# Kernel tuning notes

Measured on AMD Instinct MI355X. Metric: run time of the kernel, lower is better.

The kernel has to match this reference:

```python
import jax, jax.numpy as jnp
import numpy as np

IMG_H = 800
IMG_W = 800
LEVEL_HW = [(200, 200), (100, 100), (50, 50), (25, 25), (13, 13)]
SIZES = [32.0, 64.0, 128.0, 256.0, 512.0]
RATIOS = np.array([0.5, 1.0, 2.0])
PRE_NMS = 1000     # rpn_pre_nms_top_n_test
POST_NMS = 1000    # rpn_post_nms_top_n_test
NMS_THRESH = 0.7
MIN_SIZE = 1e-3
BBOX_CLAMP = float(np.log(1000.0 / 16.0))  # torchvision BoxCoder clamp


def _make_anchors():
    """torchvision AnchorGenerator: 3 anchors/location, (h,w,a)-major order."""
    per_level = []
    for (H, W), size in zip(LEVEL_HW, SIZES):
        h_r = np.sqrt(RATIOS)
        w_r = 1.0 / h_r
        ws = w_r * size
        hs = h_r * size
        base = np.round(np.stack([-ws, -hs, ws, hs], axis=1) / 2.0)  # [3,4]
        stride_y = IMG_H // H
        stride_x = IMG_W // W
        shift_x = np.arange(W) * stride_x
        shift_y = np.arange(H) * stride_y
        yy, xx = np.meshgrid(shift_y, shift_x, indexing='ij')
        shifts = np.stack([xx.ravel(), yy.ravel(), xx.ravel(), yy.ravel()], axis=1)
        a = (shifts[:, None, :] + base[None, :, :]).reshape(-1, 4)  # [H*W*3,4]
        per_level.append(jnp.asarray(a, jnp.float32))
    return per_level


def _conv(x, w, b, pad):
    y = jax.lax.conv_general_dilated(
        x, w, window_strides=(1, 1), padding=[(pad, pad), (pad, pad)],
        dimension_numbers=('NCHW', 'OIHW', 'NCHW'))
    return y + b[None, :, None, None]


def _rpn_forward(feats, conv_w, conv_b, cls_w, cls_b, bbox_w, bbox_b):
    anchors_l = _make_anchors()
    boxes_list, scores_list, lvls_list = [], [], []
    for lvl, f in enumerate(feats):
        t = jax.nn.relu(_conv(f, conv_w, conv_b, 1))
        logits = _conv(t, cls_w, cls_b, 0)     # [1,3,H,W]
        deltas = _conv(t, bbox_w, bbox_b, 0)   # [1,12,H,W]
        H, W = f.shape[2], f.shape[3]
        s = logits[0].transpose(1, 2, 0).reshape(-1)                       # (h,w,a)
        d = deltas[0].reshape(3, 4, H, W).transpose(2, 3, 0, 1).reshape(-1, 4)
        k = min(PRE_NMS, s.shape[0])
        topv, topi = jax.lax.top_k(s, k)
        a = anchors_l[lvl][topi]
        dd = d[topi]
        # BoxCoder.decode, weights=(1,1,1,1)
        w_ = a[:, 2] - a[:, 0]
        h_ = a[:, 3] - a[:, 1]
        cx = a[:, 0] + 0.5 * w_
        cy = a[:, 1] + 0.5 * h_
        dx, dy = dd[:, 0], dd[:, 1]
        dw = jnp.minimum(dd[:, 2], BBOX_CLAMP)
        dh = jnp.minimum(dd[:, 3], BBOX_CLAMP)
        pcx = dx * w_ + cx
        pcy = dy * h_ + cy
        pw = jnp.exp(dw) * w_
        ph = jnp.exp(dh) * h_
        bx = jnp.stack([pcx - 0.5 * pw, pcy - 0.5 * ph,
                        pcx + 0.5 * pw, pcy + 0.5 * ph], axis=1)
        boxes_list.append(bx)
        scores_list.append(topv)
        lvls_list.append(jnp.full((k,), float(lvl), jnp.float32))
    boxes = jnp.concatenate(boxes_list)    # [N,4], N=4507
    scores = jnp.concatenate(scores_list)
    lvls = jnp.concatenate(lvls_list)
    # clip to image
    boxes = jnp.stack([boxes[:, 0].clip(0.0, IMG_W), boxes[:, 1].clip(0.0, IMG_H),
                       boxes[:, 2].clip(0.0, IMG_W), boxes[:, 3].clip(0.0, IMG_H)], axis=1)
    valid = ((boxes[:, 2] - boxes[:, 0]) >= MIN_SIZE) & ((boxes[:, 3] - boxes[:, 1]) >= MIN_SIZE)
    # batched NMS: offset boxes per level so cross-level IoU is zero
    off = lvls * (IMG_W + 1.0)
    ob = boxes + off[:, None]
    N = boxes.shape[0]
    order = jnp.argsort(-scores)
    b = ob[order]
    rb = boxes[order]
    s = scores[order]
    v = valid[order]
    area = (b[:, 2] - b[:, 0]) * (b[:, 3] - b[:, 1])
    lt = jnp.maximum(b[:, None, :2], b[None, :, :2])
    rbr = jnp.minimum(b[:, None, 2:], b[None, :, 2:])
    wh = jnp.clip(rbr - lt, 0.0)
    inter = wh[..., 0] * wh[..., 1]
    iou = inter / (area[:, None] + area[None, :] - inter)  # [N,N]
    idxs = jnp.arange(N)
    def body(i, keep):
        sup = keep[i] & (iou[i] > NMS_THRESH) & (idxs > i)
        return keep & ~sup
    keep = jax.lax.fori_loop(0, N, body, v)
    final_scores = jnp.where(keep, s, -jnp.inf)
    _, ki = jax.lax.top_k(final_scores, POST_NMS)
    return rb[ki]  # [POST_NMS, 4] proposals (padded to fixed size)


def setup_inputs() -> dict:
    key = jax.random.key(0)
    ks = jax.random.split(key, 12)
    inp = {}
    for i, (name, (H, W)) in enumerate(zip(['feat0', 'feat1', 'feat2', 'feat3', 'feat4'], LEVEL_HW)):
        inp[name] = jax.random.normal(ks[i], (1, 256, H, W), jnp.float32)
    inp['conv_w'] = jax.random.normal(ks[5], (256, 256, 3, 3), jnp.float32) * 0.02
    inp['conv_b'] = jnp.zeros((256,), jnp.float32)
    inp['cls_w'] = jax.random.normal(ks[6], (3, 256, 1, 1), jnp.float32) * 0.02
    inp['cls_b'] = jnp.zeros((3,), jnp.float32)
    inp['bbox_w'] = jax.random.normal(ks[7], (12, 256, 1, 1), jnp.float32) * 0.02
    inp['bbox_b'] = jnp.zeros((12,), jnp.float32)
    return inp


def reference(feat0, feat1, feat2, feat3, feat4, conv_w, conv_b, cls_w, cls_b, bbox_w, bbox_b):
    feats = [feat0, feat1, feat2, feat3, feat4]
    return _rpn_forward(feats, conv_w, conv_b, cls_w, cls_b, bbox_w, bbox_b)
```

## Files before the change

kernel.cpp:

```cpp
#include <hip/hip_runtime.h>
#include <cmath>

typedef unsigned int u32;
typedef unsigned long long u64;
typedef _Float16 f16;
typedef _Float16 f16x8 __attribute__((ext_vector_type(8)));
typedef float f32x4 __attribute__((ext_vector_type(4)));

typedef __attribute__((address_space(1))) const unsigned int gu32;
typedef __attribute__((address_space(3))) unsigned int lu32;

#define NCAND 4507
#define WORDS 71
#define ROWS_AL (WORDS * 64)
#define TOTS 159882
#define NTILES 863
#define CONVGRID 512

__constant__ int c_W[5]      = {200, 100, 50, 25, 13};
__constant__ int c_stride[5] = {4, 8, 16, 32, 61};
__constant__ int c_Nl[5]     = {120000, 30000, 7500, 1875, 507};
__constant__ int c_soff[5]   = {0, 120000, 150000, 157500, 159375};
__constant__ int c_k[5]      = {1000, 1000, 1000, 1000, 507};

__constant__ int cv_boff[6]  = {0, 625, 794, 843, 859, 863};

struct DecParams { float b[5][3][4]; };
struct FeatPtrs { const float* p[5]; };

__device__ __forceinline__ u32 flipf(float f) {
    u32 u = __float_as_uint(f);
    return (u & 0x80000000u) ? ~u : (u | 0x80000000u);
}

constexpr size_t AL(size_t x) { return (x + 255) & ~(size_t)255; }
constexpr size_t OFF_WHI    = 0;
constexpr size_t OFF_WLO    = AL(OFF_WHI + 1179648);
constexpr size_t OFF_HEADW  = AL(OFF_WLO + 1179648);
constexpr size_t OFF_HEADB  = AL(OFF_HEADW + 3840 * 4);
constexpr size_t OFF_SCORES = AL(OFF_HEADB + 64);
constexpr size_t OFF_DELTAS = AL(OFF_SCORES + (size_t)TOTS * 4);
constexpr size_t OFF_SBOX   = AL(OFF_DELTAS + (size_t)TOTS * 16);
constexpr size_t OFF_SOB    = AL(OFF_SBOX + (size_t)NCAND * 16);
constexpr size_t OFF_SVAL   = AL(OFF_SOB + (size_t)NCAND * 16);
constexpr size_t OFF_MASK   = AL(OFF_SVAL + (size_t)NCAND * 4);
constexpr size_t OFF_KEEP   = AL(OFF_MASK + (size_t)ROWS_AL * WORDS * 8);
constexpr size_t OFF_GHIST  = AL(OFF_KEEP + WORDS * 8);
constexpr size_t OFF_CNT    = AL(OFF_GHIST + 1280 * 4);
constexpr size_t OFF_KEY    = AL(OFF_CNT + 64);

__global__ __launch_bounds__(256) void k_prep(
    const float* __restrict__ cw, const float* __restrict__ clsw,
    const float* __restrict__ clsb, const float* __restrict__ bw,
    const float* __restrict__ bb, f16* __restrict__ whi, f16* __restrict__ wlo,
    float* __restrict__ headw, float* __restrict__ headb,
    u32* __restrict__ ghist, u32* __restrict__ cnts) {
    int i = blockIdx.x * 256 + threadIdx.x;
    if (i < 589824) {
        int blk = i >> 13;
        int within = i & 8191;
        int co = within >> 5;
        int rem = within & 31;
        int slot = rem >> 3, j = rem & 7;
        int chunk = blk / 9, kk = blk - chunk * 9;
        int ky = kk / 3, kx = kk - ky * 3;
        int g = slot ^ ((co >> 1) & 3);
        int ci = (chunk << 5) | (g << 3) | j;
        float w = cw[(((co << 8) + ci) * 3 + ky) * 3 + kx];
        f16 hi = (f16)w;
        whi[i] = hi;
        wlo[i] = (f16)((w - (float)hi) * 2048.0f);
    }
    if (i < 3840) {
        int h = i >> 8, ci = i & 255;
        headw[i] = (h < 3) ? clsw[h * 256 + ci] : bw[(h - 3) * 256 + ci];
    }
    if (i < 15) headb[i] = (i < 3) ? clsb[i] : bb[i - 3];
    if (i < 1280) ghist[i] = 0;
    if (i < 16) cnts[i] = 0;
}

__global__ __launch_bounds__(512) void k_conv(
    FeatPtrs fp, const f16* __restrict__ whi, const f16* __restrict__ wlo,
    const float* __restrict__ convb, const float* __restrict__ headw,
    const float* __restrict__ headb, float* __restrict__ scores,
    float* __restrict__ deltas, u32* __restrict__ ghist) {
    __shared__ float4 smq[4896];
    char* smb = (char*)smq;
    const int tid = threadIdx.x;
    const int lane = tid & 63, wv = tid >> 6;
    const int l15 = lane & 15, l4 = lane >> 4;

    int rbase0, rbase1, rbase2, rbase3;
    {
        int rr = l15 >> 3;
        rbase0 = (0 + rr) * 640; rbase1 = (2 + rr) * 640;
        rbase2 = (4 + rr) * 640; rbase3 = (6 + rr) * 640;
    }
    int colx0, colx1, colx2;
    {
        int c = lane & 7;
        int p0 = c, p1 = c + 1, p2 = c + 2;
        colx0 = p0 * 64 + ((l4 ^ ((p0 >> 1) & 3)) << 4);
        colx1 = p1 * 64 + ((l4 ^ ((p1 >> 1) & 3)) << 4);
        colx2 = p2 * 64 + ((l4 ^ ((p2 >> 1) & 3)) << 4);
    }
    const int bco0 = wv * 32 + l15, bco1 = wv * 32 + 16 + l15;
    const int boff0 = bco0 * 64 + ((l4 ^ ((bco0 >> 1) & 3)) << 4);
    const int boff1 = bco1 * 64 + ((l4 ^ ((bco1 >> 1) & 3)) << 4);

    for (int bt = blockIdx.x; bt < NTILES; bt += gridDim.x) {
        int l = 0;
#pragma unroll
        for (int q = 1; q < 5; q++) if (bt >= cv_boff[q]) l = q;
        const int H = c_W[l], W = H;
        const int soff = c_soff[l];
        const float* __restrict__ in = fp.p[l];
        const int t = bt - cv_boff[l];
        const int tilesx = (W + 7) >> 3;
        const int tx = t % tilesx, ty = t / tilesx;
        const int x0 = tx * 8, y0 = ty * 8;
        const int HW = H * W;

        f32x4 acc1[4][2], acc2[4][2];
#pragma unroll
        for (int mt = 0; mt < 4; mt++)
#pragma unroll
            for (int nt = 0; nt < 2; nt++) {
                acc1[mt][nt] = (f32x4)0.0f;
                acc2[mt][nt] = (f32x4)0.0f;
            }

        auto stagePatch = [&](int chunk) {
            const int c0 = chunk << 5;
            f16* ph = (f16*)smb;
            f16* pl = (f16*)(smb + 6400);
            for (int e = tid; e < 3200; e += 512) {
                int py = e / 320, rem = e - py * 320;
                int px = rem >> 5, ci = rem & 31;
                int gy = y0 - 1 + py, gx = x0 - 1 + px;
                float v = 0.f;
                if (gy >= 0 && gy < H && gx >= 0 && gx < W)
                    v = in[(c0 + ci) * HW + gy * W + gx];
                f16 hi = (f16)v;
                int widx = py * 320 + px * 32 + (((ci >> 3) ^ ((px >> 1) & 3)) << 3) + (ci & 7);
                ph[widx] = hi;
                pl[widx] = (f16)((v - (float)hi) * 2048.0f);
            }
        };
        auto issueB = [&](int sidx, int buf) {
            const char* gh = (const char*)whi + (size_t)sidx * 16384;
            const char* gl = (const char*)wlo + (size_t)sidx * 16384;
            char* dh = smb + 12800 + buf * 32768;
            char* dl = dh + 16384;
#pragma unroll
            for (int q = 0; q < 2; q++) {
                int i1 = (wv * 2 + q) * 1024;
                __builtin_amdgcn_global_load_lds((gu32*)(gh + i1 + lane * 16), (lu32*)(dh + i1), 16, 0, 0);
                __builtin_amdgcn_global_load_lds((gu32*)(gl + i1 + lane * 16), (lu32*)(dl + i1), 16, 0, 0);
            }
        };

        stagePatch(0);
        issueB(0, 0);
        __syncthreads();

        for (int chunk = 0; chunk < 8; ++chunk) {
            if (chunk) { stagePatch(chunk); __syncthreads(); }
#pragma unroll
            for (int kk = 0; kk < 9; ++kk) {
                const int s = chunk * 9 + kk;
                const int buf = s & 1;
                if (s < 71) issueB(s + 1, buf ^ 1);
                {
                    const int ky = kk / 3, kx = kk - ky * 3;
                    const int kyb = ky * 640;
                    const int cx = (kx == 0) ? colx0 : (kx == 1) ? colx1 : colx2;
                    const char* bh = smb + 12800 + buf * 32768;
                    const char* bl = bh + 16384;
                    f16x8 ah0 = *(const f16x8*)(smb + rbase0 + kyb + cx);
                    f16x8 ah1 = *(const f16x8*)(smb + rbase1 + kyb + cx);
                    f16x8 ah2 = *(const f16x8*)(smb + rbase2 + kyb + cx);
                    f16x8 ah3 = *(const f16x8*)(smb + rbase3 + kyb + cx);
                    f16x8 al0 = *(const f16x8*)(smb + 6400 + rbase0 + kyb + cx);
                    f16x8 al1 = *(const f16x8*)(smb + 6400 + rbase1 + kyb + cx);
                    f16x8 al2 = *(const f16x8*)(smb + 6400 + rbase2 + kyb + cx);
                    f16x8 al3 = *(const f16x8*)(smb + 6400 + rbase3 + kyb + cx);
#pragma unroll
                    for (int nt = 0; nt < 2; nt++) {
                        const int bo = nt ? boff1 : boff0;
                        f16x8 vbh = *(const f16x8*)(bh + bo);
                        f16x8 vbl = *(const f16x8*)(bl + bo);
                        acc1[0][nt] = __builtin_amdgcn_mfma_f32_16x16x32_f16(ah0, vbh, acc1[0][nt], 0, 0, 0);
                        acc2[0][nt] = __builtin_amdgcn_mfma_f32_16x16x32_f16(ah0, vbl, acc2[0][nt], 0, 0, 0);
                        acc2[0][nt] = __builtin_amdgcn_mfma_f32_16x16x32_f16(al0, vbh, acc2[0][nt], 0, 0, 0);
                        acc1[1][nt] = __builtin_amdgcn_mfma_f32_16x16x32_f16(ah1, vbh, acc1[1][nt], 0, 0, 0);
                        acc2[1][nt] = __builtin_amdgcn_mfma_f32_16x16x32_f16(ah1, vbl, acc2[1][nt], 0, 0, 0);
                        acc2[1][nt] = __builtin_amdgcn_mfma_f32_16x16x32_f16(al1, vbh, acc2[1][nt], 0, 0, 0);
                        acc1[2][nt] = __builtin_amdgcn_mfma_f32_16x16x32_f16(ah2, vbh, acc1[2][nt], 0, 0, 0);
                        acc2[2][nt] = __builtin_amdgcn_mfma_f32_16x16x32_f16(ah2, vbl, acc2[2][nt], 0, 0, 0);
                        acc2[2][nt] = __builtin_amdgcn_mfma_f32_16x16x32_f16(al2, vbh, acc2[2][nt], 0, 0, 0);
                        acc1[3][nt] = __builtin_amdgcn_mfma_f32_16x16x32_f16(ah3, vbh, acc1[3][nt], 0, 0, 0);
                        acc2[3][nt] = __builtin_amdgcn_mfma_f32_16x16x32_f16(ah3, vbl, acc2[3][nt], 0, 0, 0);
                        acc2[3][nt] = __builtin_amdgcn_mfma_f32_16x16x32_f16(al3, vbh, acc2[3][nt], 0, 0, 0);
                    }
                }
                __syncthreads();
            }
        }

        const float INV2048 = 4.8828125e-4f;
        {
            float cb0 = convb[bco0], cb1 = convb[bco1];
#pragma unroll
            for (int mt = 0; mt < 4; mt++)
#pragma unroll
                for (int nt = 0; nt < 2; nt++) {
                    float cb = nt ? cb1 : cb0;
#pragma unroll
                    for (int r = 0; r < 4; r++) {
                        float tv = acc1[mt][nt][r] + acc2[mt][nt][r] * INV2048 + cb;
                        acc1[mt][nt][r] = tv > 0.f ? tv : 0.f;
                    }
                }
        }

        u32* lhist = (u32*)(smb + 12800);
        for (int i = tid; i < 1280; i += 512) lhist[i] = 0;

        float* part = (float*)smb;
        for (int hc = 0; hc < 15; hc += 3) {
            float hw3[3][2];
#pragma unroll
            for (int h3 = 0; h3 < 3; h3++) {
                hw3[h3][0] = headw[(hc + h3) * 256 + bco0];
                hw3[h3][1] = headw[(hc + h3) * 256 + bco1];
            }
#pragma unroll
            for (int mt = 0; mt < 4; mt++)
#pragma unroll
                for (int r = 0; r < 4; r++) {
                    float p0 = 0.f, p1 = 0.f, p2 = 0.f;
#pragma unroll
                    for (int nt = 0; nt < 2; nt++) {
                        float tv = acc1[mt][nt][r];
                        p0 = fmaf(hw3[0][nt], tv, p0);
                        p1 = fmaf(hw3[1][nt], tv, p1);
                        p2 = fmaf(hw3[2][nt], tv, p2);
                    }
                    p0 += __shfl_xor(p0, 1); p0 += __shfl_xor(p0, 2); p0 += __shfl_xor(p0, 4); p0 += __shfl_xor(p0, 8);
                    p1 += __shfl_xor(p1, 1); p1 += __shfl_xor(p1, 2); p1 += __shfl_xor(p1, 4); p1 += __shfl_xor(p1, 8);
                    p2 += __shfl_xor(p2, 1); p2 += __shfl_xor(p2, 2); p2 += __shfl_xor(p2, 4); p2 += __shfl_xor(p2, 8);
                    if (l15 == 0) {
                        int px = mt * 16 + l4 * 4 + r;
                        part[(wv * 64 + px) * 3 + 0] = p0;
                        part[(wv * 64 + px) * 3 + 1] = p1;
                        part[(wv * 64 + px) * 3 + 2] = p2;
                    }
                }
            __syncthreads();
            if (tid < 192) {
                int px = tid / 3, h3 = tid % 3;
                int h = hc + h3;
                float sum = 0.f;
#pragma unroll
                for (int g = 0; g < 8; g++) sum += part[(g * 64 + px) * 3 + h3];
                sum += headb[h];
                int gy = y0 + (px >> 3), gx = x0 + (px & 7);
                if (gy < H && gx < W) {
                    int pix = gy * W + gx;
                    if (h < 3) {
                        scores[soff + pix * 3 + h] = sum;
                        atomicAdd(&lhist[l * 256 + (flipf(sum) >> 24)], 1u);
                    } else {
                        int ch2 = h - 3;
                        deltas[((size_t)(soff + pix * 3 + (ch2 >> 2))) * 4 + (ch2 & 3)] = sum;
                    }
                }
            }
            __syncthreads();
        }
        for (int i = tid; i < 1280; i += 512) {
            u32 v = lhist[i];
            if (v) atomicAdd(&ghist[i], v);
        }
        __syncthreads();
    }
}

__global__ __launch_bounds__(1024) void k_clsfin(
    const float* __restrict__ scores, const u32* __restrict__ ghist,
    u64* __restrict__ key, u64* __restrict__ scr1, u64* __restrict__ scr2,
    u32* __restrict__ cnts, const float* __restrict__ deltas, DecParams P,
    float* __restrict__ sboxes, float* __restrict__ sob, u32* __restrict__ svalid) {
    __shared__ u64 sk[8192];
    __shared__ u32 lh[1280];
    __shared__ u32 tiebuf[2048];
    __shared__ u32 sb0[5];
    __shared__ u32 sh_sel, sh_t1, sh_t2, sh_m, sh_last;
    const int tid = threadIdx.x;
    const int lane = tid & 63;

    for (int i = tid; i < 1280; i += 1024) lh[i] = ghist[i];
    __syncthreads();
    if (tid < 4) {
        int l = tid;
        u32 m0 = (u32)c_k[l];
        u32 cum = 0;
        for (int b = 255; b >= 0; --b) {
            u32 c = lh[l * 256 + b];
            if (cum + c >= m0) { sb0[l] = (u32)b; break; }
            cum += c;
        }
    }
    __syncthreads();
    const int gsz = gridDim.x * 1024;
    for (int i = blockIdx.x * 1024 + tid; i < TOTS; i += gsz) {
        int l = (i >= 120000) + (i >= 150000) + (i >= 157500) + (i >= 159375);
        u32 il = (u32)(i - c_soff[l]);
        u32 k32 = flipf(scores[i]);
        u32 b = k32 >> 24;
        bool sel = (l == 4) || (b > sb0[l]);
        bool tie = (l < 4) && (b == sb0[l]);
        u64 m1 = __ballot(sel);
        while (m1) {
            int ldr = __builtin_ctzll(m1);
            int lv = __shfl(l, ldr);
            u64 grp = __ballot(sel && (l == lv));
            u32 bs = 0;
            if (lane == ldr) bs = atomicAdd(&cnts[lv], (u32)__popcll(grp));
            bs = __shfl(bs, ldr);
            if (sel && l == lv) {
                u32 slot = bs + (u32)__popcll(grp & ((1ull << lane) - 1ull));
                key[lv * 1000 + slot] = ((u64)(~k32) << 32) | (u64)(((u32)lv << 24) | il);
            }
            m1 &= ~grp;
        }
        u64 m2 = __ballot(tie);
        while (m2) {
            int ldr = __builtin_ctzll(m2);
            int lv = __shfl(l, ldr);
            u64 grp = __ballot(tie && (l == lv));
            u32 bs = 0;
            if (lane == ldr) bs = atomicAdd(&cnts[8 + lv], (u32)__popcll(grp));
            bs = __shfl(bs, ldr);
            if (tie && l == lv) {
                u32 slot = bs + (u32)__popcll(grp & ((1ull << lane) - 1ull));
                scr1[c_soff[lv] + slot] = ((u64)k32 << 32) | (u64)il;
            }
            m2 &= ~grp;
        }
    }
    __threadfence();
    if (tid == 0) sh_last = (atomicAdd(&cnts[12], 1u) == gridDim.x - 1) ? 1u : 0u;
    __syncthreads();
    if (!sh_last) return;
    __threadfence();

    u32* hist = lh;
    for (int l = 0; l < 5; ++l) {
        u32 n = cnts[l];
        int base = l * 1000;
        for (u32 j = tid; j < n; j += 1024) sk[base + j] = key[base + j];
    }
    __syncthreads();
    for (int l = 0; l < 4; ++l) {
        const int off = c_soff[l], base = l * 1000;
        const u32 lshift = (u32)l << 24;
        u32 nsel = cnts[l];
        u32 m = (u32)c_k[l] - nsel;
        u32 n = cnts[8 + l];
        u64* curb = scr1 + off;
        u64* nxtb = scr2 + off;
        if (tid == 0) sh_sel = nsel;
        __syncthreads();
        for (int p = 1; p <= 3; ++p) {
            if (n == m) break;
            const int shift = 56 - 8 * p;
            for (int b = tid; b < 256; b += 1024) hist[b] = 0;
            if (tid == 0) sh_t1 = 0;
            __syncthreads();
            for (u32 j = tid; j < n; j += 1024)
                atomicAdd(&hist[(u32)(curb[j] >> shift) & 255u], 1u);
            __syncthreads();
            if (tid == 0) {
                u32 cum = 0;
                for (int b = 255; b >= 0; --b) {
                    u32 c = hist[b];
                    if (cum + c >= m) { sh_t2 = (u32)b; sh_m = m - cum; break; }
                    cum += c;
                }
            }
            __syncthreads();
            u32 bp = sh_t2; m = sh_m;
            for (u32 j = tid; j < n; j += 1024) {
                u64 e = curb[j];
                u32 b = (u32)(e >> shift) & 255u;
                bool sel = b > bp, tie = (b == bp);
                u64 msk = __ballot(sel);
                if (msk) {
                    int ldr = __builtin_ctzll(msk);
                    u32 bs = 0;
                    if (lane == ldr) bs = atomicAdd(&sh_sel, (u32)__popcll(msk));
                    bs = __shfl(bs, ldr);
                    if (sel) {
                        u32 slot = bs + (u32)__popcll(msk & ((1ull << lane) - 1ull));
                        u32 k32 = (u32)(e >> 32);
                        sk[base + slot] = ((u64)(~k32) << 32) | (u64)(lshift | (u32)(e & 0xFFFFFFu));
                    }
                }
                msk = __ballot(tie);
                if (msk) {
                    int ldr = __builtin_ctzll(msk);
                    u32 bs = 0;
                    if (lane == ldr) bs = atomicAdd(&sh_t1, (u32)__popcll(msk));
                    bs = __shfl(bs, ldr);
                    if (tie) {
                        u32 slot = bs + (u32)__popcll(msk & ((1ull << lane) - 1ull));
                        nxtb[slot] = e;
                    }
                }
            }
            __syncthreads();
            n = sh_t1;
            __syncthreads();
            u64* tmp = curb; curb = nxtb; nxtb = tmp;
        }
        u32 cs = sh_sel;
        if (n == m) {
            for (u32 j = tid; j < n; j += 1024) {
                u64 e = curb[j];
                u32 k32 = (u32)(e >> 32);
                sk[base + cs + j] = ((u64)(~k32) << 32) | (u64)(lshift | (u32)(e & 0xFFFFFFu));
            }
        } else {
            u32 kt = (u32)(curb[0] >> 32);
            u32 nc = n > 2048u ? 2048u : n;
            u32 S = 64; while (S < nc) S <<= 1;
            for (u32 j = tid; j < S; j += 1024) tiebuf[j] = 0xFFFFFFFFu;
            __syncthreads();
            for (u32 j = tid; j < nc; j += 1024) tiebuf[j] = (u32)(curb[j] & 0xFFFFFFu);
            __syncthreads();
            for (u32 ksz = 2; ksz <= S; ksz <<= 1) {
                for (u32 jj = ksz >> 1; jj > 0; jj >>= 1) {
                    for (u32 i2 = tid; i2 < S; i2 += 1024) {
                        u32 ixj = i2 ^ jj;
                        if (ixj > i2) {
                            u32 a = tiebuf[i2], b2 = tiebuf[ixj];
                            bool up = ((i2 & ksz) == 0);
                            if ((a > b2) == up) { tiebuf[i2] = b2; tiebuf[ixj] = a; }
                        }
                    }
                    __syncthreads();
                }
            }
            for (u32 j = tid; j < m; j += 1024)
                sk[base + cs + j] = ((u64)(~kt) << 32) | (u64)(lshift | tiebuf[j]);
        }
        __syncthreads();
    }
    for (int i = tid; i < 8192; i += 1024) if (i >= NCAND) sk[i] = ~0ull;
    __syncthreads();
    for (u32 ksz = 2; ksz <= 8192; ksz <<= 1) {
        for (u32 j = ksz >> 1; j > 0; j >>= 1) {
            for (u32 i = tid; i < 8192; i += 1024) {
                u32 ixj = i ^ j;
                if (ixj > i) {
                    u64 a = sk[i], b = sk[ixj];
                    bool up = ((i & ksz) == 0);
                    if ((a > b) == up) { sk[i] = b; sk[ixj] = a; }
                }
            }
            __syncthreads();
        }
    }
    const float CLAMP = 4.135166556742356f;
    for (int s = tid; s < NCAND; s += 1024) {
        u32 info = (u32)sk[s];
        int l = info >> 24, idx = info & 0xFFFFFF;
        int W = c_W[l], st = c_stride[l];
        int a = idx % 3, pix = idx / 3;
        int x = pix % W, y = pix / W;
        float ax1 = x * st + P.b[l][a][0];
        float ay1 = y * st + P.b[l][a][1];
        float ax2 = x * st + P.b[l][a][2];
        float ay2 = y * st + P.b[l][a][3];
        float w_ = ax2 - ax1, h_ = ay2 - ay1;
        float cx = ax1 + 0.5f * w_, cy = ay1 + 0.5f * h_;
        const float* d = deltas + ((size_t)(c_soff[l] + idx)) * 4;
        float dx = d[0], dy = d[1];
        float dw = fminf(d[2], CLAMP), dh = fminf(d[3], CLAMP);
        float pcx = dx * w_ + cx, pcy = dy * h_ + cy;
        float pw = expf(dw) * w_, ph = expf(dh) * h_;
        float x1 = pcx - 0.5f * pw, y1 = pcy - 0.5f * ph;
        float x2 = pcx + 0.5f * pw, y2 = pcy + 0.5f * ph;
        x1 = fminf(fmaxf(x1, 0.f), 800.f); y1 = fminf(fmaxf(y1, 0.f), 800.f);
        x2 = fminf(fmaxf(x2, 0.f), 800.f); y2 = fminf(fmaxf(y2, 0.f), 800.f);
        u32 vv = (x2 - x1 >= 0.001f && y2 - y1 >= 0.001f) ? 1u : 0u;
        float offv = (float)l * 801.0f;
        sboxes[s * 4 + 0] = x1; sboxes[s * 4 + 1] = y1;
        sboxes[s * 4 + 2] = x2; sboxes[s * 4 + 3] = y2;
        sob[s * 4 + 0] = x1 + offv; sob[s * 4 + 1] = y1 + offv;
        sob[s * 4 + 2] = x2 + offv; sob[s * 4 + 3] = y2 + offv;
        svalid[s] = vv;
    }
}

__global__ __launch_bounds__(1024) void k_maskscan(
    const float* __restrict__ sob, u64* __restrict__ mask,
    const u32* __restrict__ svalid, const float* __restrict__ sboxes,
    float* __restrict__ out, u32* __restrict__ cnts) {
    __shared__ u64 stage[2][64][WORDS];
    __shared__ u64 keep[WORDS];
    __shared__ u32 ormL[WORDS], ormH[WORDS];
    __shared__ u32 sc[1024];
    __shared__ u32 sh_last;
    const int tid = threadIdx.x;
    int gid = blockIdx.x * 1024 + tid;
    const int total = NCAND * WORDS;
    if (gid < total) {
        int i = gid / WORDS, w = gid - i * WORDS;
        float bx1 = sob[i * 4], by1 = sob[i * 4 + 1], bx2 = sob[i * 4 + 2], by2 = sob[i * 4 + 3];
        float ai = (bx2 - bx1) * (by2 - by1);
        u64 bits = 0;
        int j0 = w * 64;
        for (int b = 0; b < 64; b++) {
            int j = j0 + b;
            if (j < NCAND && j > i) {
                float cx1 = sob[j * 4], cy1 = sob[j * 4 + 1], cx2 = sob[j * 4 + 2], cy2 = sob[j * 4 + 3];
                float lt0 = fmaxf(bx1, cx1), lt1 = fmaxf(by1, cy1);
                float rb0 = fminf(bx2, cx2), rb1 = fminf(by2, cy2);
                float ww = fmaxf(rb0 - lt0, 0.f), hh = fmaxf(rb1 - lt1, 0.f);
                float inter = ww * hh;
                float aj = (cx2 - cx1) * (cy2 - cy1);
                float u = ai + aj - inter;
                float iou = inter / u;
                if (iou > 0.7f) bits |= (1ull << b);
            }
        }
        mask[(size_t)i * WORDS + w] = bits;
    }
    __threadfence();
    if (tid == 0) sh_last = (atomicAdd(&cnts[13], 1u) == gridDim.x - 1) ? 1u : 0u;
    __syncthreads();
    if (!sh_last) return;
    __threadfence();

    if (tid < WORDS) {
        u64 w0 = 0;
        for (int b = 0; b < 64; b++) {
            int idx = tid * 64 + b;
            if (idx < NCAND && svalid[idx]) w0 |= (1ull << b);
        }
        keep[tid] = w0; ormL[tid] = 0; ormH[tid] = 0;
    }
    {
        u64* s0 = &stage[0][0][0];
        for (int e = tid; e < 64 * WORDS; e += 1024) {
            int r = e / WORDS, w = e - r * WORDS;
            s0[e] = (r < NCAND) ? mask[(size_t)r * WORDS + w] : 0ull;
        }
    }
    __syncthreads();

    for (int t = 0; t < WORDS; t++) {
        const int cur = t & 1;
        u64 pf[5];
        if (t < WORDS - 1) {
            int row0 = (t + 1) * 64;
#pragma unroll
            for (int q = 0; q < 5; q++) {
                int e = tid + q * 1024;
                u64 v = 0;
                if (e < 64 * WORDS) {
                    int r = e / WORDS, w = e - r * WORDS;
                    int row = row0 + r;
                    if (row < NCAND) v = mask[(size_t)row * WORDS + w];
                }
                pf[q] = v;
            }
        }
        if (tid < 64) {
            u64 d = stage[cur][tid][t];
            u64 nz = __ballot(d != 0ull);
            u64 curk = keep[t];
            u64 pending = curk & nz;
            while (pending) {
                int b = __builtin_ctzll(pending);
                pending &= pending - 1;
                u64 mb = stage[cur][b][t];
                curk &= ~mb;
                pending &= ~mb;
            }
            if (tid == 0) keep[t] = curk;
        }
        __syncthreads();
        u64 kw = keep[t];
        int nW = WORDS - 1 - t;
        for (int task = tid; task < 64 * nW; task += 1024) {
            int r = task / nW, w = t + 1 + (task - r * nW);
            if ((kw >> r) & 1ull) {
                u64 mrow = stage[cur][r][w];
                if (mrow) {
                    atomicOr(&ormL[w], (u32)mrow);
                    atomicOr(&ormH[w], (u32)(mrow >> 32));
                }
            }
        }
        __syncthreads();
        if (tid > t && tid < WORDS) {
            keep[tid] &= ~(((u64)ormH[tid] << 32) | (u64)ormL[tid]);
            ormL[tid] = 0; ormH[tid] = 0;
        }
        if (t < WORDS - 1) {
            u64* s1 = &stage[cur ^ 1][0][0];
#pragma unroll
            for (int q = 0; q < 5; q++) {
                int e = tid + q * 1024;
                if (e < 64 * WORDS) s1[e] = pf[q];
            }
        }
        __syncthreads();
    }
    const int i0 = tid * 5;
    u32 cnt = 0;
    for (int e = 0; e < 5; e++) {
        int i = i0 + e;
        if (i < NCAND) cnt += (u32)((keep[i >> 6] >> (i & 63)) & 1ull);
    }
    sc[tid] = cnt;
    __syncthreads();
    for (int off = 1; off < 1024; off <<= 1) {
        u32 v = (tid >= off) ? sc[tid - off] : 0;
        __syncthreads();
        sc[tid] += v;
        __syncthreads();
    }
    u32 incl = sc[tid];
    u32 totalk = sc[1023];
    u32 kr = incl - cnt;
    for (int e = 0; e < 5; e++) {
        int i = i0 + e;
        if (i < NCAND) {
            bool kp = (keep[i >> 6] >> (i & 63)) & 1ull;
            if (kp) {
                if (kr < 1000u) {
                    out[kr * 4 + 0] = sboxes[i * 4 + 0];
                    out[kr * 4 + 1] = sboxes[i * 4 + 1];
                    out[kr * 4 + 2] = sboxes[i * 4 + 2];
                    out[kr * 4 + 3] = sboxes[i * 4 + 3];
                }
                kr++;
            } else {
                u32 slot = totalk + (u32)i - kr;
                if (slot < 1000u) {
                    out[slot * 4 + 0] = sboxes[i * 4 + 0];
                    out[slot * 4 + 1] = sboxes[i * 4 + 1];
                    out[slot * 4 + 2] = sboxes[i * 4 + 2];
                    out[slot * 4 + 3] = sboxes[i * 4 + 3];
                }
            }
        }
    }
}

extern "C" void kernel_launch(void* const* d_in, const int* in_sizes, int n_in,
                              void* d_out, int out_size, void* d_ws, size_t ws_size,
                              hipStream_t stream) {
    (void)in_sizes; (void)n_in; (void)out_size; (void)ws_size;
    FeatPtrs fp;
    for (int i = 0; i < 5; i++) fp.p[i] = (const float*)d_in[i];
    const float* conv_w = (const float*)d_in[5];
    const float* conv_b = (const float*)d_in[6];
    const float* cls_w  = (const float*)d_in[7];
    const float* cls_b  = (const float*)d_in[8];
    const float* bbox_w = (const float*)d_in[9];
    const float* bbox_b = (const float*)d_in[10];

    char* ws = (char*)d_ws;
    f16*   whi    = (f16*)(ws + OFF_WHI);
    f16*   wlo    = (f16*)(ws + OFF_WLO);
    float* headw  = (float*)(ws + OFF_HEADW);
    float* headb  = (float*)(ws + OFF_HEADB);
    float* scores = (float*)(ws + OFF_SCORES);
    float* deltas = (float*)(ws + OFF_DELTAS);
    float* sboxes = (float*)(ws + OFF_SBOX);
    float* sob    = (float*)(ws + OFF_SOB);
    u32*   svalid = (u32*)(ws + OFF_SVAL);
    u64*   maskp  = (u64*)(ws + OFF_MASK);
    u32*   ghist  = (u32*)(ws + OFF_GHIST);
    u32*   cnts   = (u32*)(ws + OFF_CNT);
    u64*   key    = (u64*)(ws + OFF_KEY);
    u64*   scr1   = maskp;
    u64*   scr2   = maskp + TOTS;

    k_prep<<<2304, 256, 0, stream>>>(conv_w, cls_w, cls_b, bbox_w, bbox_b,
                                     whi, wlo, headw, headb, ghist, cnts);

    k_conv<<<CONVGRID, 512, 0, stream>>>(fp, whi, wlo, conv_b, headw, headb,
                                         scores, deltas, ghist);

    DecParams dp;
    {
        const double sz[5] = {32.0, 64.0, 128.0, 256.0, 512.0};
        const double rt[3] = {0.5, 1.0, 2.0};
        for (int l = 0; l < 5; l++)
            for (int a = 0; a < 3; a++) {
                double hr = sqrt(rt[a]);
                double wr = 1.0 / hr;
                double w = wr * sz[l], h = hr * sz[l];
                dp.b[l][a][0] = (float)nearbyint(-w / 2.0);
                dp.b[l][a][1] = (float)nearbyint(-h / 2.0);
                dp.b[l][a][2] = (float)nearbyint(w / 2.0);
                dp.b[l][a][3] = (float)nearbyint(h / 2.0);
            }
    }
    k_clsfin<<<128, 1024, 0, stream>>>(scores, ghist, key, scr1, scr2, cnts,
                                       deltas, dp, sboxes, sob, svalid);
    k_maskscan<<<(NCAND * WORDS + 1023) / 1024, 1024, 0, stream>>>(
        sob, maskp, svalid, sboxes, (float*)d_out, cnts);
}
```

Measured before the change: 820.0 us.

## Read conv weight fragments directly from global memory instead of LDS double buffer

Removes the async global-to-LDS double-buffered weight staging and instead has each lane load its B fragments straight from global memory, likely served by cache. This shrinks LDS from about 78KB to about 12.8KB, which could allow more blocks per CU, and drops the per-tap barrier. In exchange every wave issues redundant global loads for the same weight slices, and load latency is no longer hidden by prefetch. The histogram scratch is moved to fit the smaller LDS allocation.

```diff
diff --git a/kernel.cpp b/kernel.cpp
--- a/kernel.cpp
+++ b/kernel.cpp
@@ -6,9 +6,6 @@
 typedef _Float16 f16;
 typedef _Float16 f16x8 __attribute__((ext_vector_type(8)));
 typedef float f32x4 __attribute__((ext_vector_type(4)));
-
-typedef __attribute__((address_space(1))) const unsigned int gu32;
-typedef __attribute__((address_space(3))) unsigned int lu32;
 
 #define NCAND 4507
 #define WORDS 71
@@ -85,7 +82,7 @@
     const float* __restrict__ convb, const float* __restrict__ headw,
     const float* __restrict__ headb, float* __restrict__ scores,
     float* __restrict__ deltas, u32* __restrict__ ghist) {
-    __shared__ float4 smq[4896];
+    __shared__ float4 smq[804];
     char* smb = (char*)smq;
     const int tid = threadIdx.x;
     const int lane = tid & 63, wv = tid >> 6;
@@ -148,64 +145,45 @@
                 pl[widx] = (f16)((v - (float)hi) * 2048.0f);
             }
         };
-        auto issueB = [&](int sidx, int buf) {
-            const char* gh = (const char*)whi + (size_t)sidx * 16384;
-            const char* gl = (const char*)wlo + (size_t)sidx * 16384;
-            char* dh = smb + 12800 + buf * 32768;
-            char* dl = dh + 16384;
-#pragma unroll
-            for (int q = 0; q < 2; q++) {
-                int i1 = (wv * 2 + q) * 1024;
-                __builtin_amdgcn_global_load_lds((gu32*)(gh + i1 + lane * 16), (lu32*)(dh + i1), 16, 0, 0);
-                __builtin_amdgcn_global_load_lds((gu32*)(gl + i1 + lane * 16), (lu32*)(dl + i1), 16, 0, 0);
-            }
-        };
-
-        stagePatch(0);
-        issueB(0, 0);
-        __syncthreads();
 
         for (int chunk = 0; chunk < 8; ++chunk) {
-            if (chunk) { stagePatch(chunk); __syncthreads(); }
+            __syncthreads();
+            stagePatch(chunk);
+            __syncthreads();
 #pragma unroll
             for (int kk = 0; kk < 9; ++kk) {
                 const int s = chunk * 9 + kk;
-                const int buf = s & 1;
-                if (s < 71) issueB(s + 1, buf ^ 1);
-                {
-                    const int ky = kk / 3, kx = kk - ky * 3;
-                    const int kyb = ky * 640;
-                    const int cx = (kx == 0) ? colx0 : (kx == 1) ? colx1 : colx2;
-                    const char* bh = smb + 12800 + buf * 32768;
-                    const char* bl = bh + 16384;
-                    f16x8 ah0 = *(const f16x8*)(smb + rbase0 + kyb + cx);
-                    f16x8 ah1 = *(const f16x8*)(smb + rbase1 + kyb + cx);
-                    f16x8 ah2 = *(const f16x8*)(smb + rbase2 + kyb + cx);
-                    f16x8 ah3 = *(const f16x8*)(smb + rbase3 + kyb + cx);
-                    f16x8 al0 = *(const f16x8*)(smb + 6400 + rbase0 + kyb + cx);
-                    f16x8 al1 = *(const f16x8*)(smb + 6400 + rbase1 + kyb + cx);
-                    f16x8 al2 = *(const f16x8*)(smb + 6400 + rbase2 + kyb + cx);
-                    f16x8 al3 = *(const f16x8*)(smb + 6400 + rbase3 + kyb + cx);
-#pragma unroll
-                    for (int nt = 0; nt < 2; nt++) {
-                        const int bo = nt ? boff1 : boff0;
-                        f16x8 vbh = *(const f16x8*)(bh + bo);
-                        f16x8 vbl = *(const f16x8*)(bl + bo);
-                        acc1[0][nt] = __builtin_amdgcn_mfma_f32_16x16x32_f16(ah0, vbh, acc1[0][nt], 0, 0, 0);
-                        acc2[0][nt] = __builtin_amdgcn_mfma_f32_16x16x32_f16(ah0, vbl, acc2[0][nt], 0, 0, 0);
-                        acc2[0][nt] = __builtin_amdgcn_mfma_f32_16x16x32_f16(al0, vbh, acc2[0][nt], 0, 0, 0);
-                        acc1[1][nt] = __builtin_amdgcn_mfma_f32_16x16x32_f16(ah1, vbh, acc1[1][nt], 0, 0, 0);
-                        acc2[1][nt] = __builtin_amdgcn_mfma_f32_16x16x32_f16(ah1, vbl, acc2[1][nt], 0, 0, 0);
-                        acc2[1][nt] = __builtin_amdgcn_mfma_f32_16x16x32_f16(al1, vbh, acc2[1][nt], 0, 0, 0);
-                        acc1[2][nt] = __builtin_amdgcn_mfma_f32_16x16x32_f16(ah2, vbh, acc1[2][nt], 0, 0, 0);
-                        acc2[2][nt] = __builtin_amdgcn_mfma_f32_16x16x32_f16(ah2, vbl, acc2[2][nt], 0, 0, 0);
-                        acc2[2][nt] = __builtin_amdgcn_mfma_f32_16x16x32_f16(al2, vbh, acc2[2][nt], 0, 0, 0);
-                        acc1[3][nt] = __builtin_amdgcn_mfma_f32_16x16x32_f16(ah3, vbh, acc1[3][nt], 0, 0, 0);
-                        acc2[3][nt] = __builtin_amdgcn_mfma_f32_16x16x32_f16(ah3, vbl, acc2[3][nt], 0, 0, 0);
-                        acc2[3][nt] = __builtin_amdgcn_mfma_f32_16x16x32_f16(al3, vbh, acc2[3][nt], 0, 0, 0);
-                    }
-                }
-                __syncthreads();
+                const int ky = kk / 3, kx = kk - ky * 3;
+                const int kyb = ky * 640;
+                const int cx = (kx == 0) ? colx0 : (kx == 1) ? colx1 : colx2;
+                const char* gbh = (const char*)whi + (size_t)s * 16384;
+                const char* gbl = (const char*)wlo + (size_t)s * 16384;
+                f16x8 ah0 = *(const f16x8*)(smb + rbase0 + kyb + cx);
+                f16x8 ah1 = *(const f16x8*)(smb + rbase1 + kyb + cx);
+                f16x8 ah2 = *(const f16x8*)(smb + rbase2 + kyb + cx);
+                f16x8 ah3 = *(const f16x8*)(smb + rbase3 + kyb + cx);
+                f16x8 al0 = *(const f16x8*)(smb + 6400 + rbase0 + kyb + cx);
+                f16x8 al1 = *(const f16x8*)(smb + 6400 + rbase1 + kyb + cx);
+                f16x8 al2 = *(const f16x8*)(smb + 6400 + rbase2 + kyb + cx);
+                f16x8 al3 = *(const f16x8*)(smb + 6400 + rbase3 + kyb + cx);
+#pragma unroll
+                for (int nt = 0; nt < 2; nt++) {
+                    const int bo = nt ? boff1 : boff0;
+                    f16x8 vbh = *(const f16x8*)(gbh + bo);
+                    f16x8 vbl = *(const f16x8*)(gbl + bo);
+                    acc1[0][nt] = __builtin_amdgcn_mfma_f32_16x16x32_f16(ah0, vbh, acc1[0][nt], 0, 0, 0);
+                    acc2[0][nt] = __builtin_amdgcn_mfma_f32_16x16x32_f16(ah0, vbl, acc2[0][nt], 0, 0, 0);
+                    acc2[0][nt] = __builtin_amdgcn_mfma_f32_16x16x32_f16(al0, vbh, acc2[0][nt], 0, 0, 0);
+                    acc1[1][nt] = __builtin_amdgcn_mfma_f32_16x16x32_f16(ah1, vbh, acc1[1][nt], 0, 0, 0);
+                    acc2[1][nt] = __builtin_amdgcn_mfma_f32_16x16x32_f16(ah1, vbl, acc2[1][nt], 0, 0, 0);
+                    acc2[1][nt] = __builtin_amdgcn_mfma_f32_16x16x32_f16(al1, vbh, acc2[1][nt], 0, 0, 0);
+                    acc1[2][nt] = __builtin_amdgcn_mfma_f32_16x16x32_f16(ah2, vbh, acc1[2][nt], 0, 0, 0);
+                    acc2[2][nt] = __builtin_amdgcn_mfma_f32_16x16x32_f16(ah2, vbl, acc2[2][nt], 0, 0, 0);
+                    acc2[2][nt] = __builtin_amdgcn_mfma_f32_16x16x32_f16(al2, vbh, acc2[2][nt], 0, 0, 0);
+                    acc1[3][nt] = __builtin_amdgcn_mfma_f32_16x16x32_f16(ah3, vbh, acc1[3][nt], 0, 0, 0);
+                    acc2[3][nt] = __builtin_amdgcn_mfma_f32_16x16x32_f16(ah3, vbl, acc2[3][nt], 0, 0, 0);
+                    acc2[3][nt] = __builtin_amdgcn_mfma_f32_16x16x32_f16(al3, vbh, acc2[3][nt], 0, 0, 0);
+                }
             }
         }
 
@@ -225,7 +203,8 @@
                 }
         }
 
-        u32* lhist = (u32*)(smb + 12800);
+        __syncthreads();
+        u32* lhist = (u32*)(smb + 6400);
         for (int i = tid; i < 1280; i += 512) lhist[i] = 0;
 
         float* part = (float*)smb;
```

Measured after the change: 867.9 us. 1.06x slower.
